# Kernel tuning notes

Measured on AMD Instinct MI355X. Metric: run time of the kernel, lower is better.

## Reference

```python
import jax, jax.numpy as jnp
import numpy as np

B, S, E, H = 8, 1024, 1024, 16
D = E // H  # per-head dim = 64
STD = 0.05  # nn.init.normal_ std used in the torch module


def setup_inputs() -> dict:
    key = jax.random.key(0)
    ks = jax.random.split(key, 9)
    inputs = jax.random.normal(ks[0], (B, S, E), dtype=jnp.float32)
    mlp_params_Q = jax.random.normal(ks[1], (B, E), dtype=jnp.float32)
    mlp_params_K = jax.random.normal(ks[2], (B, E), dtype=jnp.float32)
    W_Query = jax.random.normal(ks[3], (E, E), dtype=jnp.float32) * STD
    W_Key = jax.random.normal(ks[4], (E, E), dtype=jnp.float32) * STD
    W_Value = jax.random.normal(ks[5], (E, E), dtype=jnp.float32) * STD
    W_Out = jax.random.normal(ks[6], (E, E), dtype=jnp.float32) * STD  # nn.Linear weight [out, in]
    ln_gamma = jax.random.normal(ks[7], (E,), dtype=jnp.float32) * STD
    ln_beta = jax.random.normal(ks[8], (E,), dtype=jnp.float32) * STD
    return {"inputs": inputs, "mlp_params_Q": mlp_params_Q, "mlp_params_K": mlp_params_K,
            "W_Query": W_Query, "W_Key": W_Key, "W_Value": W_Value, "W_Out": W_Out,
            "ln_gamma": ln_gamma, "ln_beta": ln_beta}


def reference(inputs, mlp_params_Q, mlp_params_K, W_Query, W_Key, W_Value, W_Out, ln_gamma, ln_beta):
    # QKV projections: [B,S,E] @ [E,E]
    q = jnp.einsum('bse,ef->bsf', inputs, W_Query)
    k = jnp.einsum('bse,ef->bsf', inputs, W_Key)
    v = jnp.einsum('bse,ef->bsf', inputs, W_Value)
    # meta gate modulation (flag='gate', mode='QK'): per-batch channel gates, *2
    q = q * mlp_params_Q[:, None, :] * 2.0
    k = k * mlp_params_K[:, None, :] * 2.0
    # split heads: channels [h*D:(h+1)*D] -> head h (matches torch.split/stack)
    qh = q.reshape(B, S, H, D)
    kh = k.reshape(B, S, H, D)
    vh = v.reshape(B, S, H, D)
    # attention scores [B,H,S,S], scaled by sqrt(D)
    scores = jnp.einsum('bihd,bjhd->bhij', qh, kh) / jnp.sqrt(jnp.asarray(D, q.dtype))
    attn = jax.nn.softmax(scores, axis=-1)  # attn_dropout is identity at eval
    out = jnp.einsum('bhij,bjhd->bihd', attn, vh).reshape(B, S, E)  # concat heads
    # output projection (nn.Linear, no bias): x @ W.T; dropout identity at eval
    res = jnp.einsum('bse,fe->bsf', out, W_Out)
    # residual + LayerNorm(eps=1e-6)
    res = res + inputs
    mean = jnp.mean(res, axis=-1, keepdims=True)
    var = jnp.mean(jnp.square(res - mean), axis=-1, keepdims=True)
    res = (res - mean) * jax.lax.rsqrt(var + 1e-6) * ln_gamma + ln_beta
    return res
```

## Files before the change

kernel.cpp:

```cpp
#include <hip/hip_runtime.h>
#include <stdint.h>

#define Bn 8
#define Sn 1024
#define En 1024
#define Hn 16
#define Dn 64
#define Mn (Bn*Sn)

typedef unsigned short u16;
typedef _Float16 f16;
typedef _Float16 f16x8 __attribute__((ext_vector_type(8)));
typedef __fp16   h16x2 __attribute__((ext_vector_type(2)));
typedef float    f32x4 __attribute__((ext_vector_type(4)));

#define VMCNT(n) asm volatile("s_waitcnt vmcnt(" #n ")" ::: "memory")
#define CFENCE() asm volatile("" ::: "memory")

static __device__ __forceinline__ u16 f2h(float x){
  f16 h = (f16)x;
  union { f16 h; u16 u; } c; c.h = h; return c.u;
}
static __device__ __forceinline__ f32x4 mfma16(f16x8 a, f16x8 b, f32x4 c){
  return __builtin_amdgcn_mfma_f32_16x16x32_f16(a, b, c, 0, 0, 0);
}
static __device__ __forceinline__ void gl_lds16(const u16* g, u16* l){
  __builtin_amdgcn_global_load_lds((__attribute__((address_space(1))) void*)g,
                                   (__attribute__((address_space(3))) void*)l, 16, 0, 0);
}

__global__ __launch_bounds__(256) void k_cvt_x(const float* __restrict__ x,
                                               u16* __restrict__ o){
  int i = blockIdx.x*256 + threadIdx.x;
  float4 v = ((const float4*)x)[i];
  ushort4 h; h.x = f2h(v.x); h.y = f2h(v.y); h.z = f2h(v.z); h.w = f2h(v.w);
  ((ushort4*)o)[i] = h;
}

__global__ __launch_bounds__(256) void k_prep_w(const float* __restrict__ Wq,
    const float* __restrict__ Wk, const float* __restrict__ Wv,
    u16* __restrict__ wq, u16* __restrict__ wk, u16* __restrict__ wv){
  __shared__ float t[32][33];
  int tx = threadIdx.x & 31, ty = threadIdx.x >> 5;
  int bx = blockIdx.x & 31, by = blockIdx.x >> 5;
  const float* W = (blockIdx.y == 0) ? Wq : (blockIdx.y == 1) ? Wk : Wv;
  u16* D = (blockIdx.y == 0) ? wq : (blockIdx.y == 1) ? wk : wv;
  for (int i = 0; i < 32; i += 8)
    t[ty+i][tx] = W[(size_t)(by*32+ty+i)*En + bx*32+tx];
  __syncthreads();
  for (int i = 0; i < 32; i += 8)
    D[(size_t)(bx*32+ty+i)*En + by*32+tx] = f2h(t[tx][ty+i]);
}

__global__ __launch_bounds__(256) void k_conv(const float* __restrict__ w,
                                              u16* __restrict__ o){
  int i = blockIdx.x*256 + threadIdx.x;
  float4 v = ((const float4*)w)[i];
  ushort4 h; h.x = f2h(v.x); h.y = f2h(v.y); h.z = f2h(v.z); h.w = f2h(v.w);
  ((ushort4*)o)[i] = h;
}

__global__ __launch_bounds__(256) void k_gemm_qkv(
    const u16* __restrict__ A, const u16* __restrict__ Bw,
    const float* __restrict__ gQ, const float* __restrict__ gK,
    u16* __restrict__ Cq, u16* __restrict__ Ck, u16* __restrict__ Vt){
  __shared__ u16 sA[128*32], sB[128*32];
  const int t = threadIdx.x, w = t >> 6, l = t & 63;
  const int lr = l & 15, lg = l >> 4;
  const int tn = blockIdx.x % 24, tm = blockIdx.x / 24;
  const int m0 = tm*128, n0 = tn*128;
  const int wr = (w >> 1)*64, wc = (w & 1)*64;
  f32x4 acc[4][4] = {};
  for (int k0 = 0; k0 < En; k0 += 32){
    for (int c = 0; c < 2; c++){
      int ch  = c*256 + t;
      int row = ch >> 2;
      int xb  = (ch & 3) << 4;
      int col = k0 + ((xb ^ ((row & 3) << 4)) >> 1);
      int ldso = (c*256 + w*64) * 16;
      gl_lds16(A  + (size_t)(m0+row)*En + col, (u16*)((char*)sA + ldso));
      gl_lds16(Bw + (size_t)(n0+row)*En + col, (u16*)((char*)sB + ldso));
    }
    __syncthreads();
    f16x8 af[4], bf[4];
    #pragma unroll
    for (int i = 0; i < 4; i++){
      int r  = wr + i*16 + lr;
      af[i] = *(const f16x8*)((const char*)sA + r*64 + ((lg*16) ^ ((r & 3) << 4)));
      int n  = wc + i*16 + lr;
      bf[i] = *(const f16x8*)((const char*)sB + n*64 + ((lg*16) ^ ((n & 3) << 4)));
    }
    __builtin_amdgcn_s_setprio(1);
    #pragma unroll
    for (int i = 0; i < 4; i++)
      #pragma unroll
      for (int j = 0; j < 4; j++)
        acc[i][j] = mfma16(af[i], bf[j], acc[i][j]);
    __builtin_amdgcn_s_setprio(0);
    __syncthreads();
  }
  const int bb = m0 >> 10;
  const int sel = n0 >> 10;
  if (sel < 2){
    const float* gate = sel ? gK : gQ;
    const float gs = sel ? 2.0f : 0.25f*1.4426950408889634f;
    u16* C = sel ? Ck : Cq;
    #pragma unroll
    for (int j = 0; j < 4; j++){
      int col = (n0 & 1023) + wc + j*16 + lr;
      float g = gate[bb*En + col] * gs;
      #pragma unroll
      for (int i = 0; i < 4; i++){
        int mbase = m0 + wr + i*16 + lg*4;
        #pragma unroll
        for (int r = 0; r < 4; r++)
          C[(size_t)(mbase + r)*En + col] = f2h(acc[i][j][r] * g);
      }
    }
  } else {
    const int s0 = (m0 & 1023) + wr;
    #pragma unroll
    for (int j = 0; j < 4; j++){
      int nn = (n0 - 2048) + wc + j*16 + lr;
      int hh = nn >> 6, d = nn & 63;
      u16* dst = Vt + ((size_t)(bb*Hn + hh)*Dn + d)*Sn;
      #pragma unroll
      for (int i = 0; i < 4; i++){
        int ss = s0 + i*16 + lg*4;
        ushort4 pk;
        pk.x = f2h(acc[i][j][0]); pk.y = f2h(acc[i][j][1]);
        pk.z = f2h(acc[i][j][2]); pk.w = f2h(acc[i][j][3]);
        *(ushort4*)&dst[ss] = pk;
      }
    }
  }
}

__global__ __launch_bounds__(256) void k_gemm_out(
    const u16* __restrict__ A, const u16* __restrict__ Bw,
    const float* __restrict__ resid, float* __restrict__ Cf){
  __shared__ u16 sA[128*32], sB[128*32];
  const int t = threadIdx.x, w = t >> 6, l = t & 63;
  const int lr = l & 15, lg = l >> 4;
  const int tn = blockIdx.x & 7, tm = blockIdx.x >> 3;
  const int m0 = tm*128, n0 = tn*128;
  const int wr = (w >> 1)*64, wc = (w & 1)*64;
  f32x4 acc[4][4] = {};
  for (int k0 = 0; k0 < En; k0 += 32){
    for (int c = 0; c < 2; c++){
      int ch  = c*256 + t;
      int row = ch >> 2;
      int xb  = (ch & 3) << 4;
      int col = k0 + ((xb ^ ((row & 3) << 4)) >> 1);
      int ldso = (c*256 + w*64) * 16;
      gl_lds16(A  + (size_t)(m0+row)*En + col, (u16*)((char*)sA + ldso));
      gl_lds16(Bw + (size_t)(n0+row)*En + col, (u16*)((char*)sB + ldso));
    }
    __syncthreads();
    f16x8 af[4], bf[4];
    #pragma unroll
    for (int i = 0; i < 4; i++){
      int r  = wr + i*16 + lr;
      af[i] = *(const f16x8*)((const char*)sA + r*64 + ((lg*16) ^ ((r & 3) << 4)));
      int n  = wc + i*16 + lr;
      bf[i] = *(const f16x8*)((const char*)sB + n*64 + ((lg*16) ^ ((n & 3) << 4)));
    }
    __builtin_amdgcn_s_setprio(1);
    #pragma unroll
    for (int i = 0; i < 4; i++)
      #pragma unroll
      for (int j = 0; j < 4; j++)
        acc[i][j] = mfma16(af[i], bf[j], acc[i][j]);
    __builtin_amdgcn_s_setprio(0);
    __syncthreads();
  }
  #pragma unroll
  for (int j = 0; j < 4; j++){
    int col = n0 + wc + j*16 + lr;
    #pragma unroll
    for (int i = 0; i < 4; i++){
      int mbase = m0 + wr + i*16 + lg*4;
      #pragma unroll
      for (int r = 0; r < 4; r++){
        size_t o = (size_t)(mbase + r)*En + col;
        Cf[o] = acc[i][j][r] + resid[o];
      }
    }
  }
}

__global__ __launch_bounds__(512) void k_attn(
    const u16* __restrict__ qp, const u16* __restrict__ kp,
    const u16* __restrict__ vt, u16* __restrict__ outp){
  __shared__ u16 sK[2][64*64];
  __shared__ u16 sVt[2][64*64];
  __shared__ u16 sP[8][16*72];
  const int t = threadIdx.x, w = t >> 6, l = t & 63;
  const int lr = l & 15, lg = l >> 4;
  const int qt = blockIdx.x >> 7, hb = blockIdx.x & 127;
  const int h = hb & 15, b = hb >> 4;
  const int q0 = qt*128 + w*16;

  const int srow = t >> 3, slot = t & 7, jc = slot ^ (srow & 7);
  const size_t gkbase = (size_t)(b*Sn + srow)*En + h*Dn + jc*8;
  const size_t gvbase = ((size_t)(b*Hn + h)*Dn + srow)*Sn + jc*8;

#define STAGE(buf, kt_) do { \
    gl_lds16(kp + gkbase + (size_t)(kt_)*64*En, (u16*)((char*)sK[buf] + w*1024)); \
    gl_lds16(vt + gvbase + (kt_)*64,            (u16*)((char*)sVt[buf] + w*1024)); \
  } while (0)

  size_t qrow = (size_t)(b*Sn + q0 + lr)*En + h*Dn;
  f16x8 qf[2];
  #pragma unroll
  for (int ks = 0; ks < 2; ks++)
    qf[ks] = *(const f16x8*)&qp[qrow + ks*32 + lg*8];
  f32x4 accO[4] = {};
  float mrun = -1e30f, lrun = 0.f;
  u16* P = &sP[w][0];

  STAGE(0, 0);
  for (int kt = 0; kt < Sn/64; kt++){
    const int cur = kt & 1;
    if (kt < Sn/64 - 1){ STAGE(cur^1, kt+1); VMCNT(2); }
    else               { VMCNT(0); }
    __builtin_amdgcn_s_barrier();
    CFENCE();
    f32x4 s[4] = {};
    __builtin_amdgcn_s_setprio(1);
    #pragma unroll
    for (int ks = 0; ks < 2; ks++)
      #pragma unroll
      for (int jt = 0; jt < 4; jt++){
        int j  = jt*16 + lr;
        int ob = j*128 + ((ks*64 + lg*16) ^ ((j & 7) << 4));
        f16x8 kf = *(const f16x8*)((const char*)sK[cur] + ob);
        s[jt] = mfma16(kf, qf[ks], s[jt]);
      }
    __builtin_amdgcn_s_setprio(0);
    float m16 = fmaxf(fmaxf(fmaxf(s[0][0], s[0][1]), fmaxf(s[0][2], s[0][3])),
                      fmaxf(fmaxf(s[1][0], s[1][1]), fmaxf(s[1][2], s[1][3])));
    m16 = fmaxf(m16, fmaxf(fmaxf(fmaxf(s[2][0], s[2][1]), fmaxf(s[2][2], s[2][3])),
                           fmaxf(fmaxf(s[3][0], s[3][1]), fmaxf(s[3][2], s[3][3]))));
    m16 = fmaxf(m16, __shfl_xor(m16, 16));
    m16 = fmaxf(m16, __shfl_xor(m16, 32));
    bool defer = __all(m16 <= mrun + 8.0f);
    float mn, sc;
    if (defer){ mn = mrun; sc = 1.0f; }
    else { mn = fmaxf(mrun, m16); sc = exp2f(mrun - mn); mrun = mn; }
    float ps = 0.f;
    #pragma unroll
    for (int jt = 0; jt < 4; jt++){
      float p0 = exp2f(s[jt][0] - mn), p1 = exp2f(s[jt][1] - mn);
      float p2 = exp2f(s[jt][2] - mn), p3 = exp2f(s[jt][3] - mn);
      ps += (p0 + p1) + (p2 + p3);
      union { h16x2 h; uint32_t u; } ca, cb;
      ca.h = __builtin_amdgcn_cvt_pkrtz(p0, p1);
      cb.h = __builtin_amdgcn_cvt_pkrtz(p2, p3);
      uint2 pk; pk.x = ca.u; pk.y = cb.u;
      *(uint2*)&P[lr*72 + jt*16 + lg*4] = pk;
    }
    ps += __shfl_xor(ps, 16);
    ps += __shfl_xor(ps, 32);
    lrun = lrun*sc + ps;
    if (!defer){
      #pragma unroll
      for (int r = 0; r < 4; r++){
        float scq = __shfl(sc, lg*4 + r);
        accO[0][r] *= scq; accO[1][r] *= scq;
        accO[2][r] *= scq; accO[3][r] *= scq;
      }
    }
    __builtin_amdgcn_s_setprio(1);
    #pragma unroll
    for (int js = 0; js < 2; js++){
      f16x8 pa = *(const f16x8*)&P[lr*72 + js*32 + lg*8];
      #pragma unroll
      for (int dt = 0; dt < 4; dt++){
        int d  = dt*16 + lr;
        int ob = d*128 + ((lg*16 + js*64) ^ ((d & 7) << 4));
        f16x8 vb = *(const f16x8*)((const char*)sVt[cur] + ob);
        accO[dt] = mfma16(pa, vb, accO[dt]);
      }
    }
    __builtin_amdgcn_s_setprio(0);
    if (kt < Sn/64 - 1){
      CFENCE();
      __builtin_amdgcn_s_barrier();
    }
  }
#undef STAGE
  float inv = 1.0f / lrun;
  float ir[4];
  #pragma unroll
  for (int r = 0; r < 4; r++) ir[r] = __shfl(inv, lg*4 + r);
  #pragma unroll
  for (int dt = 0; dt < 4; dt++){
    int dcol = h*Dn + dt*16 + lr;
    #pragma unroll
    for (int r = 0; r < 4; r++)
      outp[(size_t)(b*Sn + q0 + lg*4 + r)*En + dcol] = f2h(accO[dt][r] * ir[r]);
  }
}

__global__ __launch_bounds__(256) void k_ln(const float* __restrict__ res,
    const float* __restrict__ gamma, const float* __restrict__ beta,
    float* __restrict__ out){
  int row = blockIdx.x, t = threadIdx.x;
  const float* r = res + (size_t)row*En;
  float4 v = ((const float4*)r)[t];
  float s = v.x + v.y + v.z + v.w;
  float q = v.x*v.x + v.y*v.y + v.z*v.z + v.w*v.w;
  for (int d = 1; d < 64; d <<= 1){ s += __shfl_xor(s, d); q += __shfl_xor(q, d); }
  __shared__ float ss[4], sq[4];
  int w = t >> 6, l = t & 63;
  if (l == 0){ ss[w] = s; sq[w] = q; }
  __syncthreads();
  s = ss[0] + ss[1] + ss[2] + ss[3];
  q = sq[0] + sq[1] + sq[2] + sq[3];
  float mean = s * (1.f/En);
  float var  = q * (1.f/En) - mean*mean;
  float rs   = rsqrtf(var + 1e-6f);
  float4 g = ((const float4*)gamma)[t], bb = ((const float4*)beta)[t];
  float4 o;
  o.x = (v.x - mean)*rs*g.x + bb.x;
  o.y = (v.y - mean)*rs*g.y + bb.y;
  o.z = (v.z - mean)*rs*g.z + bb.z;
  o.w = (v.w - mean)*rs*g.w + bb.w;
  ((float4*)(out + (size_t)row*En))[t] = o;
}

extern "C" void kernel_launch(void* const* d_in, const int* in_sizes, int n_in,
                              void* d_out, int out_size, void* d_ws, size_t ws_size,
                              hipStream_t stream){
  (void)in_sizes; (void)n_in; (void)out_size; (void)ws_size;
  const float* X     = (const float*)d_in[0];
  const float* gQ    = (const float*)d_in[1];
  const float* gK    = (const float*)d_in[2];
  const float* Wq    = (const float*)d_in[3];
  const float* Wk    = (const float*)d_in[4];
  const float* Wv    = (const float*)d_in[5];
  const float* Wo    = (const float*)d_in[6];
  const float* gamma = (const float*)d_in[7];
  const float* beta  = (const float*)d_in[8];
  float* out = (float*)d_out;

  char* ws = (char*)d_ws;
  const size_t sz = (size_t)Mn*En*2;
  u16* xh = (u16*)(ws + 0*sz);
  u16* qh = (u16*)(ws + 1*sz);
  u16* kh = (u16*)(ws + 2*sz);
  u16* vb = (u16*)(ws + 3*sz);
  u16* ao = (u16*)(ws + 4*sz);
  float* res = (float*)(ws + 0*sz);
  u16* wq = (u16*)(ws + 5*sz);
  u16* wk = wq + (size_t)En*En;
  u16* wv = wk + (size_t)En*En;
  u16* wo = wv + (size_t)En*En;

  k_cvt_x<<<Mn*En/1024, 256, 0, stream>>>(X, xh);
  k_prep_w<<<dim3((En/32)*(En/32), 3), 256, 0, stream>>>(Wq, Wk, Wv, wq, wk, wv);
  k_conv<<<En*En/1024, 256, 0, stream>>>(Wo, wo);
  k_gemm_qkv<<<(Mn/128)*(3*En/128), 256, 0, stream>>>(xh, wq, gQ, gK, qh, kh, vb);
  k_attn<<<(Sn/128)*Hn*Bn, 512, 0, stream>>>(qh, kh, vb, ao);
  k_gemm_out<<<(Mn/128)*(En/128), 256, 0, stream>>>(ao, wo, X, res);
  k_ln<<<Mn, 256, 0, stream>>>(res, gamma, beta, out);
}
```

Baseline: 297.0 us.

## Double-buffer GEMM LDS tiles, fuse prep kernels, store residual in fp16

Merges the three conversion/transpose kernels into one launch. Adds LDS double buffering to both GEMMs so the next K-tile's global-to-LDS load is issued before the current tile's MFMAs. Stores the residual sum as fp16 to halve the traffic between the out-projection and LayerNorm, and uses raw v_exp_f32 in softmax. The attention loop swaps its explicit vmcnt waits and raw barriers for __syncthreads. The GEMMs issue the next tile's async loads without a wait before reading the current buffer, which may rely on __syncthreads' implicit waitcnt and could stall on the prefetch or race. The fp16 residual costs precision.

```diff
diff --git a/kernel.cpp b/kernel.cpp
--- a/kernel.cpp
+++ b/kernel.cpp
@@ -14,13 +14,16 @@
 typedef __fp16   h16x2 __attribute__((ext_vector_type(2)));
 typedef float    f32x4 __attribute__((ext_vector_type(4)));
 
-#define VMCNT(n) asm volatile("s_waitcnt vmcnt(" #n ")" ::: "memory")
-#define CFENCE() asm volatile("" ::: "memory")
-
 static __device__ __forceinline__ u16 f2h(float x){
   f16 h = (f16)x;
   union { f16 h; u16 u; } c; c.h = h; return c.u;
 }
+static __device__ __forceinline__ float h2f(u16 u){
+  union { u16 u; f16 h; } c; c.u = u; return (float)c.h;
+}
+static __device__ __forceinline__ float fexp2(float x){
+  float r; asm("v_exp_f32 %0, %1" : "=v"(r) : "v"(x)); return r;
+}
 static __device__ __forceinline__ f32x4 mfma16(f16x8 a, f16x8 b, f32x4 c){
   return __builtin_amdgcn_mfma_f32_16x16x32_f16(a, b, c, 0, 0, 0);
 }
@@ -29,66 +32,70 @@
                                    (__attribute__((address_space(3))) void*)l, 16, 0, 0);
 }
 
-__global__ __launch_bounds__(256) void k_cvt_x(const float* __restrict__ x,
-                                               u16* __restrict__ o){
-  int i = blockIdx.x*256 + threadIdx.x;
-  float4 v = ((const float4*)x)[i];
-  ushort4 h; h.x = f2h(v.x); h.y = f2h(v.y); h.z = f2h(v.z); h.w = f2h(v.w);
-  ((ushort4*)o)[i] = h;
-}
-
-__global__ __launch_bounds__(256) void k_prep_w(const float* __restrict__ Wq,
-    const float* __restrict__ Wk, const float* __restrict__ Wv,
-    u16* __restrict__ wq, u16* __restrict__ wk, u16* __restrict__ wv){
-  __shared__ float t[32][33];
-  int tx = threadIdx.x & 31, ty = threadIdx.x >> 5;
-  int bx = blockIdx.x & 31, by = blockIdx.x >> 5;
-  const float* W = (blockIdx.y == 0) ? Wq : (blockIdx.y == 1) ? Wk : Wv;
-  u16* D = (blockIdx.y == 0) ? wq : (blockIdx.y == 1) ? wk : wv;
-  for (int i = 0; i < 32; i += 8)
-    t[ty+i][tx] = W[(size_t)(by*32+ty+i)*En + bx*32+tx];
-  __syncthreads();
-  for (int i = 0; i < 32; i += 8)
-    D[(size_t)(bx*32+ty+i)*En + by*32+tx] = f2h(t[tx][ty+i]);
-}
-
-__global__ __launch_bounds__(256) void k_conv(const float* __restrict__ w,
-                                              u16* __restrict__ o){
-  int i = blockIdx.x*256 + threadIdx.x;
-  float4 v = ((const float4*)w)[i];
-  ushort4 h; h.x = f2h(v.x); h.y = f2h(v.y); h.z = f2h(v.z); h.w = f2h(v.w);
-  ((ushort4*)o)[i] = h;
+__global__ __launch_bounds__(256) void k_prep(const float* __restrict__ X,
+    const float* __restrict__ Wq, const float* __restrict__ Wk,
+    const float* __restrict__ Wv, const float* __restrict__ Wo,
+    u16* __restrict__ xh, u16* __restrict__ wq, u16* __restrict__ wk,
+    u16* __restrict__ wv, u16* __restrict__ wo){
+  __shared__ float tsh[32][33];
+  const int bid = blockIdx.x, tid = threadIdx.x;
+  if (bid < 9216){
+    const float* src = (bid < 8192) ? X : Wo;
+    u16* dst = (bid < 8192) ? xh : wo;
+    int i = (bid < 8192 ? bid : bid - 8192)*256 + tid;
+    float4 v = ((const float4*)src)[i];
+    ushort4 h; h.x = f2h(v.x); h.y = f2h(v.y); h.z = f2h(v.z); h.w = f2h(v.w);
+    ((ushort4*)dst)[i] = h;
+  } else {
+    int pb = bid - 9216;
+    int sel = pb >> 10, inner = pb & 1023;
+    int bx = inner & 31, by = inner >> 5;
+    int tx = tid & 31, ty = tid >> 5;
+    const float* W = (sel == 0) ? Wq : (sel == 1) ? Wk : Wv;
+    u16* D = (sel == 0) ? wq : (sel == 1) ? wk : wv;
+    for (int i = 0; i < 32; i += 8)
+      tsh[ty+i][tx] = W[(size_t)(by*32+ty+i)*En + bx*32+tx];
+    __syncthreads();
+    for (int i = 0; i < 32; i += 8)
+      D[(size_t)(bx*32+ty+i)*En + by*32+tx] = f2h(tsh[tx][ty+i]);
+  }
 }
 
 __global__ __launch_bounds__(256) void k_gemm_qkv(
     const u16* __restrict__ A, const u16* __restrict__ Bw,
     const float* __restrict__ gQ, const float* __restrict__ gK,
     u16* __restrict__ Cq, u16* __restrict__ Ck, u16* __restrict__ Vt){
-  __shared__ u16 sA[128*32], sB[128*32];
+  __shared__ u16 sA[2*128*32], sB[2*128*32];
   const int t = threadIdx.x, w = t >> 6, l = t & 63;
   const int lr = l & 15, lg = l >> 4;
   const int tn = blockIdx.x % 24, tm = blockIdx.x / 24;
   const int m0 = tm*128, n0 = tn*128;
   const int wr = (w >> 1)*64, wc = (w & 1)*64;
   f32x4 acc[4][4] = {};
-  for (int k0 = 0; k0 < En; k0 += 32){
-    for (int c = 0; c < 2; c++){
-      int ch  = c*256 + t;
-      int row = ch >> 2;
-      int xb  = (ch & 3) << 4;
-      int col = k0 + ((xb ^ ((row & 3) << 4)) >> 1);
-      int ldso = (c*256 + w*64) * 16;
-      gl_lds16(A  + (size_t)(m0+row)*En + col, (u16*)((char*)sA + ldso));
-      gl_lds16(Bw + (size_t)(n0+row)*En + col, (u16*)((char*)sB + ldso));
-    }
-    __syncthreads();
+
+#define GSTAGE(buf, k0_) do { \
+    for (int c = 0; c < 2; c++){ \
+      int ch  = c*256 + t; \
+      int row = ch >> 2; \
+      int xb  = (ch & 3) << 4; \
+      int col = (k0_) + ((xb ^ ((row & 3) << 4)) >> 1); \
+      int ldso = (buf)*8192 + (c*256 + w*64)*16; \
+      gl_lds16(A  + (size_t)(m0+row)*En + col, (u16*)((char*)sA + ldso)); \
+      gl_lds16(Bw + (size_t)(n0+row)*En + col, (u16*)((char*)sB + ldso)); \
+    } } while (0)
+
+  GSTAGE(0, 0);
+  __syncthreads();
+  for (int kt = 0; kt < En/32; kt++){
+    const int cur = kt & 1;
+    if (kt < En/32 - 1) GSTAGE(cur^1, (kt+1)*32);
     f16x8 af[4], bf[4];
     #pragma unroll
     for (int i = 0; i < 4; i++){
       int r  = wr + i*16 + lr;
-      af[i] = *(const f16x8*)((const char*)sA + r*64 + ((lg*16) ^ ((r & 3) << 4)));
+      af[i] = *(const f16x8*)((const char*)sA + cur*8192 + r*64 + ((lg*16) ^ ((r & 3) << 4)));
       int n  = wc + i*16 + lr;
-      bf[i] = *(const f16x8*)((const char*)sB + n*64 + ((lg*16) ^ ((n & 3) << 4)));
+      bf[i] = *(const f16x8*)((const char*)sB + cur*8192 + n*64 + ((lg*16) ^ ((n & 3) << 4)));
     }
     __builtin_amdgcn_s_setprio(1);
     #pragma unroll
@@ -99,6 +106,7 @@
     __builtin_amdgcn_s_setprio(0);
     __syncthreads();
   }
+#undef GSTAGE
   const int bb = m0 >> 10;
   const int sel = n0 >> 10;
   if (sel < 2){
@@ -138,32 +146,38 @@
 
 __global__ __launch_bounds__(256) void k_gemm_out(
     const u16* __restrict__ A, const u16* __restrict__ Bw,
-    const float* __restrict__ resid, float* __restrict__ Cf){
-  __shared__ u16 sA[128*32], sB[128*32];
+    const float* __restrict__ resid, u16* __restrict__ resh){
+  __shared__ u16 sA[2*128*32], sB[2*128*32];
   const int t = threadIdx.x, w = t >> 6, l = t & 63;
   const int lr = l & 15, lg = l >> 4;
   const int tn = blockIdx.x & 7, tm = blockIdx.x >> 3;
   const int m0 = tm*128, n0 = tn*128;
   const int wr = (w >> 1)*64, wc = (w & 1)*64;
   f32x4 acc[4][4] = {};
-  for (int k0 = 0; k0 < En; k0 += 32){
-    for (int c = 0; c < 2; c++){
-      int ch  = c*256 + t;
-      int row = ch >> 2;
-      int xb  = (ch & 3) << 4;
-      int col = k0 + ((xb ^ ((row & 3) << 4)) >> 1);
-      int ldso = (c*256 + w*64) * 16;
-      gl_lds16(A  + (size_t)(m0+row)*En + col, (u16*)((char*)sA + ldso));
-      gl_lds16(Bw + (size_t)(n0+row)*En + col, (u16*)((char*)sB + ldso));
-    }
-    __syncthreads();
+
+#define GSTAGE(buf, k0_) do { \
+    for (int c = 0; c < 2; c++){ \
+      int ch  = c*256 + t; \
+      int row = ch >> 2; \
+      int xb  = (ch & 3) << 4; \
+      int col = (k0_) + ((xb ^ ((row & 3) << 4)) >> 1); \
+      int ldso = (buf)*8192 + (c*256 + w*64)*16; \
+      gl_lds16(A  + (size_t)(m0+row)*En + col, (u16*)((char*)sA + ldso)); \
+      gl_lds16(Bw + (size_t)(n0+row)*En + col, (u16*)((char*)sB + ldso)); \
+    } } while (0)
+
+  GSTAGE(0, 0);
+  __syncthreads();
+  for (int kt = 0; kt < En/32; kt++){
+    const int cur = kt & 1;
+    if (kt < En/32 - 1) GSTAGE(cur^1, (kt+1)*32);
     f16x8 af[4], bf[4];
     #pragma unroll
     for (int i = 0; i < 4; i++){
       int r  = wr + i*16 + lr;
-      af[i] = *(const f16x8*)((const char*)sA + r*64 + ((lg*16) ^ ((r & 3) << 4)));
+      af[i] = *(const f16x8*)((const char*)sA + cur*8192 + r*64 + ((lg*16) ^ ((r & 3) << 4)));
       int n  = wc + i*16 + lr;
-      bf[i] = *(const f16x8*)((const char*)sB + n*64 + ((lg*16) ^ ((n & 3) << 4)));
+      bf[i] = *(const f16x8*)((const char*)sB + cur*8192 + n*64 + ((lg*16) ^ ((n & 3) << 4)));
     }
     __builtin_amdgcn_s_setprio(1);
     #pragma unroll
@@ -174,6 +188,7 @@
     __builtin_amdgcn_s_setprio(0);
     __syncthreads();
   }
+#undef GSTAGE
   #pragma unroll
   for (int j = 0; j < 4; j++){
     int col = n0 + wc + j*16 + lr;
@@ -183,7 +198,7 @@
       #pragma unroll
       for (int r = 0; r < 4; r++){
         size_t o = (size_t)(mbase + r)*En + col;
-        Cf[o] = acc[i][j][r] + resid[o];
+        resh[o] = f2h(acc[i][j][r] + resid[o]);
       }
     }
   }
@@ -220,12 +235,10 @@
   u16* P = &sP[w][0];
 
   STAGE(0, 0);
+  __syncthreads();
   for (int kt = 0; kt < Sn/64; kt++){
     const int cur = kt & 1;
-    if (kt < Sn/64 - 1){ STAGE(cur^1, kt+1); VMCNT(2); }
-    else               { VMCNT(0); }
-    __builtin_amdgcn_s_barrier();
-    CFENCE();
+    if (kt < Sn/64 - 1) STAGE(cur^1, kt+1);
     f32x4 s[4] = {};
     __builtin_amdgcn_s_setprio(1);
     #pragma unroll
@@ -247,12 +260,12 @@
     bool defer = __all(m16 <= mrun + 8.0f);
     float mn, sc;
     if (defer){ mn = mrun; sc = 1.0f; }
-    else { mn = fmaxf(mrun, m16); sc = exp2f(mrun - mn); mrun = mn; }
+    else { mn = fmaxf(mrun, m16); sc = fexp2(mrun - mn); mrun = mn; }
     float ps = 0.f;
     #pragma unroll
     for (int jt = 0; jt < 4; jt++){
-      float p0 = exp2f(s[jt][0] - mn), p1 = exp2f(s[jt][1] - mn);
-      float p2 = exp2f(s[jt][2] - mn), p3 = exp2f(s[jt][3] - mn);
+      float p0 = fexp2(s[jt][0] - mn), p1 = fexp2(s[jt][1] - mn);
+      float p2 = fexp2(s[jt][2] - mn), p3 = fexp2(s[jt][3] - mn);
       ps += (p0 + p1) + (p2 + p3);
       union { h16x2 h; uint32_t u; } ca, cb;
       ca.h = __builtin_amdgcn_cvt_pkrtz(p0, p1);
@@ -284,10 +297,7 @@
       }
     }
     __builtin_amdgcn_s_setprio(0);
-    if (kt < Sn/64 - 1){
-      CFENCE();
-      __builtin_amdgcn_s_barrier();
-    }
+    __syncthreads();
   }
 #undef STAGE
   float inv = 1.0f / lrun;
@@ -303,14 +313,15 @@
   }
 }
 
-__global__ __launch_bounds__(256) void k_ln(const float* __restrict__ res,
+__global__ __launch_bounds__(256) void k_ln(const u16* __restrict__ res,
     const float* __restrict__ gamma, const float* __restrict__ beta,
     float* __restrict__ out){
   int row = blockIdx.x, t = threadIdx.x;
-  const float* r = res + (size_t)row*En;
-  float4 v = ((const float4*)r)[t];
-  float s = v.x + v.y + v.z + v.w;
-  float q = v.x*v.x + v.y*v.y + v.z*v.z + v.w*v.w;
+  const u16* r = res + (size_t)row*En;
+  ushort4 v4 = ((const ushort4*)r)[t];
+  float vx = h2f(v4.x), vy = h2f(v4.y), vz = h2f(v4.z), vw = h2f(v4.w);
+  float s = vx + vy + vz + vw;
+  float q = vx*vx + vy*vy + vz*vz + vw*vw;
   for (int d = 1; d < 64; d <<= 1){ s += __shfl_xor(s, d); q += __shfl_xor(q, d); }
   __shared__ float ss[4], sq[4];
   int w = t >> 6, l = t & 63;
@@ -323,10 +334,10 @@
   float rs   = rsqrtf(var + 1e-6f);
   float4 g = ((const float4*)gamma)[t], bb = ((const float4*)beta)[t];
   float4 o;
-  o.x = (v.x - mean)*rs*g.x + bb.x;
-  o.y = (v.y - mean)*rs*g.y + bb.y;
-  o.z = (v.z - mean)*rs*g.z + bb.z;
-  o.w = (v.w - mean)*rs*g.w + bb.w;
+  o.x = (vx - mean)*rs*g.x + bb.x;
+  o.y = (vy - mean)*rs*g.y + bb.y;
+  o.z = (vz - mean)*rs*g.z + bb.z;
+  o.w = (vw - mean)*rs*g.w + bb.w;
   ((float4*)(out + (size_t)row*En))[t] = o;
 }
 
@@ -352,15 +363,13 @@
   u16* kh = (u16*)(ws + 2*sz);
   u16* vb = (u16*)(ws + 3*sz);
   u16* ao = (u16*)(ws + 4*sz);
-  float* res = (float*)(ws + 0*sz);
+  u16* res = (u16*)(ws + 0*sz);
   u16* wq = (u16*)(ws + 5*sz);
   u16* wk = wq + (size_t)En*En;
   u16* wv = wk + (size_t)En*En;
   u16* wo = wv + (size_t)En*En;
 
-  k_cvt_x<<<Mn*En/1024, 256, 0, stream>>>(X, xh);
-  k_prep_w<<<dim3((En/32)*(En/32), 3), 256, 0, stream>>>(Wq, Wk, Wv, wq, wk, wv);
-  k_conv<<<En*En/1024, 256, 0, stream>>>(Wo, wo);
+  k_prep<<<12288, 256, 0, stream>>>(X, Wq, Wk, Wv, Wo, xh, wq, wk, wv, wo);
   k_gemm_qkv<<<(Mn/128)*(3*En/128), 256, 0, stream>>>(xh, wq, gQ, gK, qh, kh, vb);
   k_attn<<<(Sn/128)*Hn*Bn, 512, 0, stream>>>(qh, kh, vb, ao);
   k_gemm_out<<<(Mn/128)*(En/128), 256, 0, stream>>>(ao, wo, X, res);
```

Result: faster. 276.7 us (-6.8%).
